# Optimization experiments

Measured on AMD Instinct MI355X. Metric: run time of the kernel, lower is better.

Reference implementation:

```python
import jax, jax.numpy as jnp
import numpy as np

D_EMB = 1024
N_HEAD = 16
D_K = D_EMB // N_HEAD


def setup_inputs() -> dict:
    key = jax.random.key(0)
    ks = jax.random.split(key, 11)
    B, S = 2, 2048
    s = 1.0 / np.sqrt(D_EMB)
    inp = {
        'Q': jax.random.normal(ks[0], (B, S, D_EMB), jnp.float32),
        'K': jax.random.normal(ks[1], (B, S, D_EMB), jnp.float32),
        'V': jax.random.normal(ks[2], (B, S, D_EMB), jnp.float32),
        'W_Q': jax.random.normal(ks[3], (D_EMB, D_EMB), jnp.float32) * s,
        'b_Q': jax.random.normal(ks[4], (D_EMB,), jnp.float32) * s,
        'W_K': jax.random.normal(ks[5], (D_EMB, D_EMB), jnp.float32) * s,
        'b_K': jax.random.normal(ks[6], (D_EMB,), jnp.float32) * s,
        'W_V': jax.random.normal(ks[7], (D_EMB, D_EMB), jnp.float32) * s,
        'b_V': jax.random.normal(ks[8], (D_EMB,), jnp.float32) * s,
        'W_O': jax.random.normal(ks[9], (D_EMB, D_EMB), jnp.float32) * s,
        'b_O': jax.random.normal(ks[10], (D_EMB,), jnp.float32) * s,
    }
    return inp


def _heads(x):
    # [B, S, D] -> [B, H, S, d_k]
    B, S, _ = x.shape
    return x.reshape(B, S, N_HEAD, D_K).transpose(0, 2, 1, 3)


def reference(Q, K, V, W_Q, b_Q, W_K, b_K, W_V, b_V, W_O, b_O):
    q = _heads(Q @ W_Q.T + b_Q)
    k = _heads(K @ W_K.T + b_K)
    v = _heads(V @ W_V.T + b_V)
    scale = 1.0 / jnp.sqrt(jnp.asarray(D_K, q.dtype))
    scores = jnp.einsum('bhqd,bhkd->bhqk', q, k) * scale  # [B,H,S,S]
    probs = jax.nn.softmax(scores, axis=-1)
    attn = jnp.einsum('bhqk,bhkd->bhqd', probs, v)
    B, H, S, d = attn.shape
    attn = attn.transpose(0, 2, 1, 3).reshape(B, S, H * d)
    return attn @ W_O.T + b_O
```

## Files before the change

### kernel.cpp

```cpp
#include <hip/hip_runtime.h>
#include <cstdint>
#include <cstddef>

#define S_LEN 2048
#define NH    16
#define DKH   64
#define DEMB  1024
#define MTOT  4096

typedef float f32x4 __attribute__((ext_vector_type(4)));
typedef __bf16 bf16x8 __attribute__((ext_vector_type(8)));
typedef unsigned short u16;
typedef unsigned int u32;
typedef u16 u16x8 __attribute__((ext_vector_type(8)));
typedef u16 u16x4 __attribute__((ext_vector_type(4)));
typedef u32 u32x2 __attribute__((ext_vector_type(2)));

static __device__ __forceinline__ u16 f2bf(float f) {
  u32 u = __builtin_bit_cast(u32, f);
  u += 0x7fffu + ((u >> 16) & 1u);
  return (u16)(u >> 16);
}
static __device__ __forceinline__ bf16x8 ldfrag(const u16* p) {
  return __builtin_bit_cast(bf16x8, *(const u16x8*)p);
}
static __device__ __forceinline__ f32x4 mfma16(bf16x8 a, bf16x8 b, f32x4 c) {
  return __builtin_amdgcn_mfma_f32_16x16x32_bf16(a, b, c, 0, 0, 0);
}
static __device__ __forceinline__ void gl2lds16(const void* g, void* l) {
  __builtin_amdgcn_global_load_lds((__attribute__((address_space(1))) void*)g,
                                   (__attribute__((address_space(3))) void*)l,
                                   16, 0, 0);
}
static __device__ __forceinline__ u32 pkbf(float hi, float lo) {
  u32 a = __builtin_bit_cast(u32, hi) + 0x8000u;
  u32 b = __builtin_bit_cast(u32, lo) + 0x8000u;
  return __builtin_amdgcn_perm(a, b, 0x07060302u);
}

#define SCL_Q (0.125f * 1.44269504088896340736f)

__global__ __launch_bounds__(256) void cvt_bf16(const float* __restrict__ s,
                                                u16* __restrict__ d, int n) {
  int i = (blockIdx.x * 256 + threadIdx.x) * 4;
  if (i >= n) return;
  f32x4 f = *(const f32x4*)(s + i);
  u16x4 o;
  o[0] = f2bf(f[0]); o[1] = f2bf(f[1]); o[2] = f2bf(f[2]); o[3] = f2bf(f[3]);
  *(u16x4*)(d + i) = o;
}

__global__ __launch_bounds__(256) void qkv_gemm(
    const u16* __restrict__ qin, const u16* __restrict__ kin,
    const u16* __restrict__ vin, const u16* __restrict__ W,
    const float* __restrict__ bq, const float* __restrict__ bk,
    const float* __restrict__ bv,
    u16* __restrict__ qh, u16* __restrict__ kh, u16* __restrict__ vt) {
  __shared__ __align__(16) u16 sA[128 * 32];
  __shared__ __align__(16) u16 sB[128 * 32];
  const int t = threadIdx.x;
  const int l = t & 63, w = t >> 6;
  const int ll = l & 15, lg = l >> 4;
  const int nb = blockIdx.x;
  const int mb = blockIdx.y;
  const int which = nb >> 3;
  const u16* A = (which == 0) ? qin : ((which == 1) ? kin : vin);
  const int wr = (w >> 1) * 64, wc = (w & 1) * 64;

  f32x4 acc[4][4] = {};

  for (int kt = 0; kt < 32; ++kt) {
    const int k0 = kt * 32;
    __syncthreads();
#pragma unroll
    for (int i = 0; i < 2; ++i) {
      const int c = i * 256 + t;
      const int row = c >> 2;
      const int gc = (c & 3) ^ ((row >> 1) & 3);
      gl2lds16(A + (size_t)(mb * 128 + row) * DEMB + k0 + gc * 8, &sA[c * 8]);
      gl2lds16(W + (size_t)(nb * 128 + row) * DEMB + k0 + gc * 8, &sB[c * 8]);
    }
    __syncthreads();

    bf16x8 af[4], bfr[4];
#pragma unroll
    for (int i2 = 0; i2 < 4; ++i2) {
      const int row = wr + i2 * 16 + ll;
      af[i2] = ldfrag(&sA[row * 32 + (lg ^ ((row >> 1) & 3)) * 8]);
    }
#pragma unroll
    for (int j2 = 0; j2 < 4; ++j2) {
      const int row = wc + j2 * 16 + ll;
      bfr[j2] = ldfrag(&sB[row * 32 + (lg ^ ((row >> 1) & 3)) * 8]);
    }
#pragma unroll
    for (int i2 = 0; i2 < 4; ++i2)
#pragma unroll
      for (int j2 = 0; j2 < 4; ++j2)
        acc[i2][j2] = mfma16(af[i2], bfr[j2], acc[i2][j2]);
  }

  const float* bias = (which == 0) ? bq : ((which == 1) ? bk : bv);
  const int b = (mb * 128) >> 11;

  if (which == 2) {
#pragma unroll
    for (int j2 = 0; j2 < 4; ++j2) {
      const int nl = (nb * 128 + wc + j2 * 16 + ll) & 1023;
      const int h = nl >> 6, dk = nl & 63;
      const float bb = bias[nl];
      u16* base = vt + ((size_t)((b * NH + h) * DKH + dk)) * S_LEN;
#pragma unroll
      for (int i2 = 0; i2 < 4; ++i2) {
        const int s = (mb * 128 + wr + i2 * 16 + lg * 4) & 2047;
        u16x4 pk;
#pragma unroll
        for (int r = 0; r < 4; ++r) pk[r] = f2bf(acc[i2][j2][r] + bb);
        *(u16x4*)&base[s] = pk;
      }
    }
  } else {
    u16* outp = (which == 0) ? qh : kh;
    const float scl = (which == 0) ? SCL_Q : 1.0f;
#pragma unroll
    for (int j2 = 0; j2 < 4; ++j2) {
      const int nl = (nb * 128 + wc + j2 * 16 + ll) & 1023;
      const int h = nl >> 6, dk = nl & 63;
      const float bb = bias[nl];
#pragma unroll
      for (int i2 = 0; i2 < 4; ++i2) {
#pragma unroll
        for (int r = 0; r < 4; ++r) {
          const int s = (mb * 128 + wr + i2 * 16 + lg * 4 + r) & 2047;
          const float val = (acc[i2][j2][r] + bb) * scl;
          outp[((size_t)((b * NH + h) * S_LEN + s)) * DKH + dk] = f2bf(val);
        }
      }
    }
  }
}

__global__ __launch_bounds__(256) void attn_kernel(
    const u16* __restrict__ qh, const u16* __restrict__ kh,
    const u16* __restrict__ vt, u16* __restrict__ ctx) {
  __shared__ __align__(16) u16 sK[128 * 64];
  __shared__ __align__(16) u16 sV[64 * 128];
  __shared__ __align__(16) u16 sP[4][2][16 * 68];
  const int t = threadIdx.x;
  const int l = t & 63, w = t >> 6;
  const int ll = l & 15, lg = l >> 4;
  const int q_blk = blockIdx.x * 128;
  const int bh = blockIdx.y;

  bf16x8 aq[2][2];
#pragma unroll
  for (int qt = 0; qt < 2; ++qt) {
    const u16* qbase = qh + ((size_t)bh * S_LEN + q_blk + w * 32 + qt * 16 + ll) * DKH;
    aq[qt][0] = ldfrag(qbase + lg * 8);
    aq[qt][1] = ldfrag(qbase + 32 + lg * 8);
  }

  f32x4 oT[2][4] = {};
  float l_part[2] = {0.f, 0.f};

  u16* sP0 = &sP[w][0][0];
  u16* sP1 = &sP[w][1][0];

  for (int kt = 0; kt < 16; ++kt) {
    __syncthreads();
#pragma unroll
    for (int i = 0; i < 4; ++i) {
      const int c = i * 256 + t;
      {
        const int row = c >> 3, gc = (c & 7) ^ (row & 7);
        gl2lds16(kh + ((size_t)bh * S_LEN + kt * 128 + row) * DKH + gc * 8,
                 &sK[c * 8]);
      }
      {
        const int row = c >> 4, gc = (c & 15) ^ (row & 15);
        gl2lds16(vt + ((size_t)bh * DKH + row) * S_LEN + kt * 128 + gc * 8,
                 &sV[c * 8]);
      }
    }
    __syncthreads();

#pragma unroll
    for (int h = 0; h < 2; ++h) {
#pragma unroll
      for (int kbl = 0; kbl < 4; ++kbl) {
        const int kb = h * 4 + kbl;
        const int krow = kb * 16 + ll;
        const bf16x8 ak0 = ldfrag(&sK[krow * 64 + (lg ^ (ll & 7)) * 8]);
        const bf16x8 ak1 = ldfrag(&sK[krow * 64 + ((4 + lg) ^ (ll & 7)) * 8]);
        f32x4 s0 = {}, s1 = {};
        s0 = mfma16(ak0, aq[0][0], s0);
        s0 = mfma16(ak1, aq[0][1], s0);
        s1 = mfma16(ak0, aq[1][0], s1);
        s1 = mfma16(ak1, aq[1][1], s1);
        const int poff = ll * 68 + kbl * 16 + lg * 4;
        {
          const float p0 = __builtin_amdgcn_exp2f(s0[0]);
          const float p1 = __builtin_amdgcn_exp2f(s0[1]);
          const float p2 = __builtin_amdgcn_exp2f(s0[2]);
          const float p3 = __builtin_amdgcn_exp2f(s0[3]);
          l_part[0] += (p0 + p1) + (p2 + p3);
          u32x2 pk; pk[0] = pkbf(p1, p0); pk[1] = pkbf(p3, p2);
          *(u32x2*)&sP0[poff] = pk;
        }
        {
          const float p0 = __builtin_amdgcn_exp2f(s1[0]);
          const float p1 = __builtin_amdgcn_exp2f(s1[1]);
          const float p2 = __builtin_amdgcn_exp2f(s1[2]);
          const float p3 = __builtin_amdgcn_exp2f(s1[3]);
          l_part[1] += (p0 + p1) + (p2 + p3);
          u32x2 pk; pk[0] = pkbf(p1, p0); pk[1] = pkbf(p3, p2);
          *(u32x2*)&sP1[poff] = pk;
        }
      }

      bf16x8 bp[2][2];
#pragma unroll
      for (int fl = 0; fl < 2; ++fl) {
        const int off = ll * 68 + fl * 32 + lg * 8;
        const u16x4 lo0 = *(const u16x4*)&sP0[off];
        const u16x4 hi0 = *(const u16x4*)&sP0[off + 4];
        bp[0][fl] = __builtin_bit_cast(bf16x8,
            __builtin_shufflevector(lo0, hi0, 0, 1, 2, 3, 4, 5, 6, 7));
        const u16x4 lo1 = *(const u16x4*)&sP1[off];
        const u16x4 hi1 = *(const u16x4*)&sP1[off + 4];
        bp[1][fl] = __builtin_bit_cast(bf16x8,
            __builtin_shufflevector(lo1, hi1, 0, 1, 2, 3, 4, 5, 6, 7));
      }
#pragma unroll
      for (int nt = 0; nt < 4; ++nt) {
        const int vrow = nt * 16 + ll;
#pragma unroll
        for (int fl = 0; fl < 2; ++fl) {
          const int fg = h * 2 + fl;
          const bf16x8 av = ldfrag(&sV[vrow * 128 + ((fg * 4 + lg) ^ ll) * 8]);
          oT[0][nt] = mfma16(av, bp[0][fl], oT[0][nt]);
          oT[1][nt] = mfma16(av, bp[1][fl], oT[1][nt]);
        }
      }
    }
  }

  const int b = bh >> 4, h = bh & 15;
#pragma unroll
  for (int qt = 0; qt < 2; ++qt) {
    float lv = l_part[qt];
    lv += __shfl_xor(lv, 16, 64);
    lv += __shfl_xor(lv, 32, 64);
    const float inv = 1.0f / lv;
    const int srow = q_blk + w * 32 + qt * 16 + ll;
#pragma unroll
    for (int nt = 0; nt < 4; ++nt) {
      u16x4 o;
#pragma unroll
      for (int r = 0; r < 4; ++r) o[r] = f2bf(oT[qt][nt][r] * inv);
      *(u16x4*)&ctx[((size_t)((b * S_LEN + srow) * NH + h)) * DKH + nt * 16 + lg * 4] = o;
    }
  }
}

__global__ __launch_bounds__(256) void out_gemm(
    const u16* __restrict__ Am, const u16* __restrict__ W,
    const float* __restrict__ bo, float* __restrict__ out) {
  __shared__ __align__(16) u16 sA[64 * 64];
  __shared__ __align__(16) u16 sB[64 * 64];
  const int t = threadIdx.x;
  const int l = t & 63, w = t >> 6;
  const int ll = l & 15, lg = l >> 4;
  const int nb = blockIdx.x;
  const int mb = blockIdx.y;
  const int wr = (w >> 1) * 32, wc = (w & 1) * 32;

  f32x4 acc[2][2] = {};
  for (int kt = 0; kt < 16; ++kt) {
    const int k0 = kt * 64;
    __syncthreads();
#pragma unroll
    for (int i = 0; i < 2; ++i) {
      const int c = i * 256 + t;
      const int row = c >> 3;
      const int gc = (c & 7) ^ (row & 7);
      gl2lds16(Am + (size_t)(mb * 64 + row) * DEMB + k0 + gc * 8, &sA[c * 8]);
      gl2lds16(W + (size_t)(nb * 64 + row) * DEMB + k0 + gc * 8, &sB[c * 8]);
    }
    __syncthreads();
#pragma unroll
    for (int sub = 0; sub < 2; ++sub) {
      bf16x8 af[2], bfr[2];
#pragma unroll
      for (int i2 = 0; i2 < 2; ++i2) {
        const int row = wr + i2 * 16 + ll;
        af[i2] = ldfrag(&sA[row * 64 + ((sub * 4 + lg) ^ (row & 7)) * 8]);
      }
#pragma unroll
      for (int j2 = 0; j2 < 2; ++j2) {
        const int row = wc + j2 * 16 + ll;
        bfr[j2] = ldfrag(&sB[row * 64 + ((sub * 4 + lg) ^ (row & 7)) * 8]);
      }
#pragma unroll
      for (int i2 = 0; i2 < 2; ++i2)
#pragma unroll
        for (int j2 = 0; j2 < 2; ++j2)
          acc[i2][j2] = mfma16(af[i2], bfr[j2], acc[i2][j2]);
    }
  }

#pragma unroll
  for (int j2 = 0; j2 < 2; ++j2) {
    const int ncol = nb * 64 + wc + j2 * 16 + ll;
    const float bb = bo[ncol];
#pragma unroll
    for (int i2 = 0; i2 < 2; ++i2) {
#pragma unroll
      for (int r = 0; r < 4; ++r) {
        const int mrow = mb * 64 + wr + i2 * 16 + lg * 4 + r;
        out[(size_t)mrow * DEMB + ncol] = acc[i2][j2][r] + bb;
      }
    }
  }
}

extern "C" void kernel_launch(void* const* d_in, const int* in_sizes, int n_in,
                              void* d_out, int out_size, void* d_ws,
                              size_t ws_size, hipStream_t stream) {
  (void)in_sizes; (void)n_in; (void)out_size; (void)ws_size;
  const float* Q  = (const float*)d_in[0];
  const float* K  = (const float*)d_in[1];
  const float* V  = (const float*)d_in[2];
  const float* WQ = (const float*)d_in[3];
  const float* bQ = (const float*)d_in[4];
  const float* WK = (const float*)d_in[5];
  const float* bK = (const float*)d_in[6];
  const float* WV = (const float*)d_in[7];
  const float* bV = (const float*)d_in[8];
  const float* WO = (const float*)d_in[9];
  const float* bO = (const float*)d_in[10];
  float* out = (float*)d_out;

  u16* ws   = (u16*)d_ws;
  u16* Wqkv = ws;
  u16* Wo   = Wqkv + 3072 * 1024;
  u16* qin  = Wo + 1024 * 1024;
  u16* kin  = qin + (size_t)MTOT * DEMB;
  u16* vin  = kin + (size_t)MTOT * DEMB;
  u16* qh   = vin + (size_t)MTOT * DEMB;
  u16* kh   = qh + 32 * 2048 * 64;
  u16* vt   = kh + 32 * 2048 * 64;
  u16* ctx  = vt + 32 * 2048 * 64;

  const int WN = DEMB * DEMB;
  const int AN = MTOT * DEMB;
  cvt_bf16<<<WN / 1024, 256, 0, stream>>>(WQ, Wqkv, WN);
  cvt_bf16<<<WN / 1024, 256, 0, stream>>>(WK, Wqkv + WN, WN);
  cvt_bf16<<<WN / 1024, 256, 0, stream>>>(WV, Wqkv + 2 * WN, WN);
  cvt_bf16<<<WN / 1024, 256, 0, stream>>>(WO, Wo, WN);
  cvt_bf16<<<AN / 1024, 256, 0, stream>>>(Q, qin, AN);
  cvt_bf16<<<AN / 1024, 256, 0, stream>>>(K, kin, AN);
  cvt_bf16<<<AN / 1024, 256, 0, stream>>>(V, vin, AN);

  qkv_gemm<<<dim3(24, 32), 256, 0, stream>>>(qin, kin, vin, Wqkv, bQ, bK, bV,
                                             qh, kh, vt);
  attn_kernel<<<dim3(16, 32), 256, 0, stream>>>(qh, kh, vt, ctx);
  out_gemm<<<dim3(16, 64), 256, 0, stream>>>(ctx, Wo, bO, out);
}
```

Baseline: 250.1 us.

## Split attention over key halves and merge partial outputs in a new kernel

Measured after the change: 251.3 us. Within noise of the previous version (+0.5%).

```diff
diff --git a/kernel.cpp b/kernel.cpp
--- a/kernel.cpp
+++ b/kernel.cpp
@@ -20,6 +20,9 @@
   u32 u = __builtin_bit_cast(u32, f);
   u += 0x7fffu + ((u >> 16) & 1u);
   return (u16)(u >> 16);
+}
+static __device__ __forceinline__ float bf2f(u16 b) {
+  return __builtin_bit_cast(float, ((u32)b) << 16);
 }
 static __device__ __forceinline__ bf16x8 ldfrag(const u16* p) {
   return __builtin_bit_cast(bf16x8, *(const u16x8*)p);
@@ -142,14 +145,17 @@
 
 __global__ __launch_bounds__(256) void attn_kernel(
     const u16* __restrict__ qh, const u16* __restrict__ kh,
-    const u16* __restrict__ vt, u16* __restrict__ ctx) {
-  __shared__ __align__(16) u16 sK[128 * 64];
-  __shared__ __align__(16) u16 sV[64 * 128];
+    const u16* __restrict__ vt, u16* __restrict__ opart,
+    float* __restrict__ lpart) {
+  __shared__ __align__(16) u16 sK[64 * 64];
+  __shared__ __align__(16) u16 sV[64 * 64];
   __shared__ __align__(16) u16 sP[4][2][16 * 68];
   const int t = threadIdx.x;
   const int l = t & 63, w = t >> 6;
   const int ll = l & 15, lg = l >> 4;
-  const int q_blk = blockIdx.x * 128;
+  const int qb = blockIdx.x >> 1;
+  const int ks = blockIdx.x & 1;
+  const int q_blk = qb * 128;
   const int bh = blockIdx.y;
 
   bf16x8 aq[2][2];
@@ -167,100 +173,108 @@
   u16* sP1 = &sP[w][1][0];
 
   for (int kt = 0; kt < 16; ++kt) {
-    __syncthreads();
-#pragma unroll
-    for (int i = 0; i < 4; ++i) {
+    const int kb0 = ks * 1024 + kt * 64;
+    __syncthreads();
+#pragma unroll
+    for (int i = 0; i < 2; ++i) {
       const int c = i * 256 + t;
+      const int row = c >> 3, gc = (c & 7) ^ (row & 7);
+      gl2lds16(kh + ((size_t)bh * S_LEN + kb0 + row) * DKH + gc * 8,
+               &sK[c * 8]);
+      gl2lds16(vt + ((size_t)bh * DKH + row) * S_LEN + kb0 + gc * 8,
+               &sV[c * 8]);
+    }
+    __syncthreads();
+
+#pragma unroll
+    for (int kbl = 0; kbl < 4; ++kbl) {
+      const int krow = kbl * 16 + ll;
+      const bf16x8 ak0 = ldfrag(&sK[krow * 64 + (lg ^ (ll & 7)) * 8]);
+      const bf16x8 ak1 = ldfrag(&sK[krow * 64 + ((4 + lg) ^ (ll & 7)) * 8]);
+      f32x4 s0 = {}, s1 = {};
+      s0 = mfma16(ak0, aq[0][0], s0);
+      s0 = mfma16(ak1, aq[0][1], s0);
+      s1 = mfma16(ak0, aq[1][0], s1);
+      s1 = mfma16(ak1, aq[1][1], s1);
+      const int poff = ll * 68 + kbl * 16 + lg * 4;
       {
-        const int row = c >> 3, gc = (c & 7) ^ (row & 7);
-        gl2lds16(kh + ((size_t)bh * S_LEN + kt * 128 + row) * DKH + gc * 8,
-                 &sK[c * 8]);
+        const float p0 = __builtin_amdgcn_exp2f(s0[0]);
+        const float p1 = __builtin_amdgcn_exp2f(s0[1]);
+        const float p2 = __builtin_amdgcn_exp2f(s0[2]);
+        const float p3 = __builtin_amdgcn_exp2f(s0[3]);
+        l_part[0] += (p0 + p1) + (p2 + p3);
+        u32x2 pk; pk[0] = pkbf(p1, p0); pk[1] = pkbf(p3, p2);
+        *(u32x2*)&sP0[poff] = pk;
       }
       {
-        const int row = c >> 4, gc = (c & 15) ^ (row & 15);
-        gl2lds16(vt + ((size_t)bh * DKH + row) * S_LEN + kt * 128 + gc * 8,
-                 &sV[c * 8]);
-      }
-    }
-    __syncthreads();
-
-#pragma unroll
-    for (int h = 0; h < 2; ++h) {
-#pragma unroll
-      for (int kbl = 0; kbl < 4; ++kbl) {
-        const int kb = h * 4 + kbl;
-        const int krow = kb * 16 + ll;
-        const bf16x8 ak0 = ldfrag(&sK[krow * 64 + (lg ^ (ll & 7)) * 8]);
-        const bf16x8 ak1 = ldfrag(&sK[krow * 64 + ((4 + lg) ^ (ll & 7)) * 8]);
-        f32x4 s0 = {}, s1 = {};
-        s0 = mfma16(ak0, aq[0][0], s0);
-        s0 = mfma16(ak1, aq[0][1], s0);
-        s1 = mfma16(ak0, aq[1][0], s1);
-        s1 = mfma16(ak1, aq[1][1], s1);
-        const int poff = ll * 68 + kbl * 16 + lg * 4;
-        {
-          const float p0 = __builtin_amdgcn_exp2f(s0[0]);
-          const float p1 = __builtin_amdgcn_exp2f(s0[1]);
-          const float p2 = __builtin_amdgcn_exp2f(s0[2]);
-          const float p3 = __builtin_amdgcn_exp2f(s0[3]);
-          l_part[0] += (p0 + p1) + (p2 + p3);
-          u32x2 pk; pk[0] = pkbf(p1, p0); pk[1] = pkbf(p3, p2);
-          *(u32x2*)&sP0[poff] = pk;
-        }
-        {
-          const float p0 = __builtin_amdgcn_exp2f(s1[0]);
-          const float p1 = __builtin_amdgcn_exp2f(s1[1]);
-          const float p2 = __builtin_amdgcn_exp2f(s1[2]);
-          const float p3 = __builtin_amdgcn_exp2f(s1[3]);
-          l_part[1] += (p0 + p1) + (p2 + p3);
-          u32x2 pk; pk[0] = pkbf(p1, p0); pk[1] = pkbf(p3, p2);
-          *(u32x2*)&sP1[poff] = pk;
-        }
-      }
-
-      bf16x8 bp[2][2];
+        const float p0 = __builtin_amdgcn_exp2f(s1[0]);
+        const float p1 = __builtin_amdgcn_exp2f(s1[1]);
+        const float p2 = __builtin_amdgcn_exp2f(s1[2]);
+        const float p3 = __builtin_amdgcn_exp2f(s1[3]);
+        l_part[1] += (p0 + p1) + (p2 + p3);
+        u32x2 pk; pk[0] = pkbf(p1, p0); pk[1] = pkbf(p3, p2);
+        *(u32x2*)&sP1[poff] = pk;
+      }
+    }
+
+    bf16x8 bp[2][2];
+#pragma unroll
+    for (int fl = 0; fl < 2; ++fl) {
+      const int off = ll * 68 + fl * 32 + lg * 8;
+      const u16x4 lo0 = *(const u16x4*)&sP0[off];
+      const u16x4 hi0 = *(const u16x4*)&sP0[off + 4];
+      bp[0][fl] = __builtin_bit_cast(bf16x8,
+          __builtin_shufflevector(lo0, hi0, 0, 1, 2, 3, 4, 5, 6, 7));
+      const u16x4 lo1 = *(const u16x4*)&sP1[off];
+      const u16x4 hi1 = *(const u16x4*)&sP1[off + 4];
+      bp[1][fl] = __builtin_bit_cast(bf16x8,
+          __builtin_shufflevector(lo1, hi1, 0, 1, 2, 3, 4, 5, 6, 7));
+    }
+#pragma unroll
+    for (int nt = 0; nt < 4; ++nt) {
+      const int vrow = nt * 16 + ll;
 #pragma unroll
       for (int fl = 0; fl < 2; ++fl) {
-        const int off = ll * 68 + fl * 32 + lg * 8;
-        const u16x4 lo0 = *(const u16x4*)&sP0[off];
-        const u16x4 hi0 = *(const u16x4*)&sP0[off + 4];
-        bp[0][fl] = __builtin_bit_cast(bf16x8,
-            __builtin_shufflevector(lo0, hi0, 0, 1, 2, 3, 4, 5, 6, 7));
-        const u16x4 lo1 = *(const u16x4*)&sP1[off];
-        const u16x4 hi1 = *(const u16x4*)&sP1[off + 4];
-        bp[1][fl] = __builtin_bit_cast(bf16x8,
-            __builtin_shufflevector(lo1, hi1, 0, 1, 2, 3, 4, 5, 6, 7));
-      }
-#pragma unroll
-      for (int nt = 0; nt < 4; ++nt) {
-        const int vrow = nt * 16 + ll;
-#pragma unroll
-        for (int fl = 0; fl < 2; ++fl) {
-          const int fg = h * 2 + fl;
-          const bf16x8 av = ldfrag(&sV[vrow * 128 + ((fg * 4 + lg) ^ ll) * 8]);
-          oT[0][nt] = mfma16(av, bp[0][fl], oT[0][nt]);
-          oT[1][nt] = mfma16(av, bp[1][fl], oT[1][nt]);
-        }
-      }
-    }
-  }
-
-  const int b = bh >> 4, h = bh & 15;
+        const bf16x8 av = ldfrag(&sV[vrow * 64 + ((fl * 4 + lg) ^ (vrow & 7)) * 8]);
+        oT[0][nt] = mfma16(av, bp[0][fl], oT[0][nt]);
+        oT[1][nt] = mfma16(av, bp[1][fl], oT[1][nt]);
+      }
+    }
+  }
+
 #pragma unroll
   for (int qt = 0; qt < 2; ++qt) {
     float lv = l_part[qt];
     lv += __shfl_xor(lv, 16, 64);
     lv += __shfl_xor(lv, 32, 64);
-    const float inv = 1.0f / lv;
     const int srow = q_blk + w * 32 + qt * 16 + ll;
+    u16* obase = opart + (((size_t)(ks * 32 + bh)) * S_LEN + srow) * DKH;
 #pragma unroll
     for (int nt = 0; nt < 4; ++nt) {
       u16x4 o;
 #pragma unroll
-      for (int r = 0; r < 4; ++r) o[r] = f2bf(oT[qt][nt][r] * inv);
-      *(u16x4*)&ctx[((size_t)((b * S_LEN + srow) * NH + h)) * DKH + nt * 16 + lg * 4] = o;
-    }
-  }
+      for (int r = 0; r < 4; ++r) o[r] = f2bf(oT[qt][nt][r]);
+      *(u16x4*)&obase[nt * 16 + lg * 4] = o;
+    }
+    if (lg == 0) lpart[(ks * 32 + bh) * S_LEN + srow] = lv;
+  }
+}
+
+__global__ __launch_bounds__(256) void merge_ctx(
+    const u16* __restrict__ op, const float* __restrict__ lp,
+    u16* __restrict__ ctx) {
+  const int idx = blockIdx.x * 256 + threadIdx.x;
+  const int dk8 = idx & 7;
+  const int q = (idx >> 3) & 2047;
+  const int bh = idx >> 14;
+  const float inv = 1.0f / (lp[bh * S_LEN + q] + lp[(32 + bh) * S_LEN + q]);
+  const u16x8 a = *(const u16x8*)&op[((size_t)bh * S_LEN + q) * DKH + dk8 * 8];
+  const u16x8 c = *(const u16x8*)&op[((size_t)(32 + bh) * S_LEN + q) * DKH + dk8 * 8];
+  u16x8 o;
+#pragma unroll
+  for (int r = 0; r < 8; ++r) o[r] = f2bf((bf2f(a[r]) + bf2f(c[r])) * inv);
+  const int b = bh >> 4, h = bh & 15;
+  *(u16x8*)&ctx[((size_t)((b * S_LEN + q) * NH + h)) * DKH + dk8 * 8] = o;
 }
 
 __global__ __launch_bounds__(256) void out_gemm(
@@ -351,6 +365,8 @@
   u16* kh   = qh + 32 * 2048 * 64;
   u16* vt   = kh + 32 * 2048 * 64;
   u16* ctx  = vt + 32 * 2048 * 64;
+  u16* opart   = qin;
+  float* lpart = (float*)Wqkv;
 
   const int WN = DEMB * DEMB;
   const int AN = MTOT * DEMB;
@@ -364,6 +380,7 @@
 
   qkv_gemm<<<dim3(24, 32), 256, 0, stream>>>(qin, kin, vin, Wqkv, bQ, bK, bV,
                                              qh, kh, vt);
-  attn_kernel<<<dim3(16, 32), 256, 0, stream>>>(qh, kh, vt, ctx);
+  attn_kernel<<<dim3(32, 32), 256, 0, stream>>>(qh, kh, vt, opart, lpart);
+  merge_ctx<<<2048, 256, 0, stream>>>(opart, lpart, ctx);
   out_gemm<<<dim3(16, 64), 256, 0, stream>>>(ctx, Wo, bO, out);
 }
```
